# Optimization experiments

Hardware: AMD Instinct MI355X
Metric: run time of the kernel (lower is better)

## Reference

```python
import jax, jax.numpy as jnp
import numpy as np

N = 50000      # nodes
E = 800000     # edges
P = 200000     # link pairs
D_IN = 128     # input_dim
F_NUM = 128    # filter_num
OUT = 2        # out_dim
K = 10         # APPNP propagation steps
ALPHA = 0.1    # teleport prob


def setup_inputs() -> dict:
    key = jax.random.key(0)
    ks = jax.random.split(key, 9)
    x = jax.random.normal(ks[0], (N, D_IN), dtype=jnp.float32)
    edge_index = jax.random.randint(ks[1], (2, E), 0, N)
    index = jax.random.randint(ks[2], (P, 2), 0, N)
    s1 = 1.0 / np.sqrt(D_IN)
    s2 = 1.0 / np.sqrt(F_NUM)
    s3 = 1.0 / np.sqrt(2 * F_NUM)
    W1 = jax.random.uniform(ks[3], (F_NUM, D_IN), minval=-s1, maxval=s1)
    b1 = jax.random.uniform(ks[4], (F_NUM,), minval=-s1, maxval=s1)
    W2 = jax.random.uniform(ks[5], (F_NUM, F_NUM), minval=-s2, maxval=s2)
    b2 = jax.random.uniform(ks[6], (F_NUM,), minval=-s2, maxval=s2)
    W3 = jax.random.uniform(ks[7], (OUT, 2 * F_NUM), minval=-s3, maxval=s3)
    b3 = jax.random.uniform(ks[8], (OUT,), minval=-s3, maxval=s3)
    return {"x": x, "edge_index": edge_index, "index": index,
            "W1": W1, "b1": b1, "W2": W2, "b2": b2, "W3": W3, "b3": b3}


def _gcn_norm(edge_index, num_nodes):
    # PyG gcn_norm: add self-loops, sym norm D^{-1/2} (A+I) D^{-1/2}
    src, dst = edge_index[0], edge_index[1]
    loop = jnp.arange(num_nodes, dtype=src.dtype)
    src = jnp.concatenate([src, loop])
    dst = jnp.concatenate([dst, loop])
    deg = jax.ops.segment_sum(jnp.ones_like(src, dtype=jnp.float32), dst,
                              num_segments=num_nodes)
    dinv = jnp.where(deg > 0, jax.lax.rsqrt(deg), 0.0)
    norm = dinv[src] * dinv[dst]  # [E+N]
    return src, dst, norm


def _appnp(x, src, dst, norm, num_nodes):
    # h_{k+1} = (1-alpha) * A_hat h_k + alpha * x0
    def step(h, _):
        agg = jax.ops.segment_sum(norm[:, None] * h[src], dst,
                                  num_segments=num_nodes)
        return (1.0 - ALPHA) * agg + ALPHA * x, None
    h, _ = jax.lax.scan(step, x, None, length=K)
    return h


def reference(x, edge_index, index, W1, b1, W2, b2, W3, b3):
    num_nodes = x.shape[0]
    src, dst, norm = _gcn_norm(edge_index, num_nodes)
    h = x @ W1.T + b1                      # [N, F]
    h = jax.nn.relu(_appnp(h, src, dst, norm, num_nodes))
    h = h @ W2.T + b2                      # [N, F]
    h = jax.nn.relu(_appnp(h, src, dst, norm, num_nodes))
    feat = jnp.concatenate([h[index[:, 0]], h[index[:, 1]]], axis=-1)  # [P, 2F]
    out = feat @ W3.T + b3                 # [P, OUT]
    return jax.nn.log_softmax(out, axis=1)
```

## Files before the change

### kernel.cpp

```cpp
#include <hip/hip_runtime.h>
#include <math.h>

#define NN 50000
#define NE 800000
#define NP 200000
#define NF 128
#define NEDGE_TOT (NE + NN)
#define NBLK 196
#define NBK 64
#define DPB 782
#define BKCAP 16384
#define EPB 2048

typedef __attribute__((ext_vector_type(8))) short short8;
typedef __attribute__((ext_vector_type(4))) float float4v;
typedef __attribute__((ext_vector_type(2))) _Float16 h2;

__device__ __forceinline__ float bf_lo(unsigned u) { return __uint_as_float(u << 16); }
__device__ __forceinline__ float bf_hi(unsigned u) { return __uint_as_float(u & 0xffff0000u); }
__device__ __forceinline__ unsigned short f2bf(float f) {
    unsigned u = __float_as_uint(f);
    return (unsigned short)((u + 0x7fffu + ((u >> 16) & 1u)) >> 16);
}
__device__ __forceinline__ unsigned pack2bf(float a, float b) {
    return (unsigned)f2bf(a) | ((unsigned)f2bf(b) << 16);
}

__device__ __forceinline__ h2 u2h2(unsigned u) {
    union { unsigned u; h2 h; } c; c.u = u; return c.h;
}
__device__ __forceinline__ unsigned h22u(h2 h) {
    union { unsigned u; h2 h; } c; c.h = h; return c.u;
}
__device__ __forceinline__ float h_lo(unsigned u) { return (float)u2h2(u).x; }
__device__ __forceinline__ float h_hi(unsigned u) { return (float)u2h2(u).y; }
__device__ __forceinline__ unsigned pack2h(float a, float b) {
    h2 h; h.x = (_Float16)a; h.y = (_Float16)b; return h22u(h);
}

__global__ __launch_bounds__(256) void init_cnt_k(int* __restrict__ cnt) {
    int i = blockIdx.x * 256 + threadIdx.x;
    if (i < NN) cnt[i] = 1;
}

__global__ __launch_bounds__(256) void count_k(const int* __restrict__ ei,
                                               int* __restrict__ cnt) {
    int e = blockIdx.x * 256 + threadIdx.x;
    if (e < NE) atomicAdd(&cnt[ei[NE + e]], 1);
}

__global__ __launch_bounds__(256) void scan_reduce_k(const int* __restrict__ cnt,
                                                     int* __restrict__ bsum,
                                                     float* __restrict__ dinv) {
    __shared__ int s[256];
    int t = threadIdx.x;
    int idx = blockIdx.x * 256 + t;
    int v = (idx < NN) ? cnt[idx] : 0;
    if (idx < NN) dinv[idx] = rsqrtf((float)v);
    s[t] = v;
    __syncthreads();
    for (int off = 128; off > 0; off >>= 1) {
        if (t < off) s[t] += s[t + off];
        __syncthreads();
    }
    if (t == 0) bsum[blockIdx.x] = s[0];
}

__global__ __launch_bounds__(256) void scan_bsums_k(const int* __restrict__ bsum,
                                                    int* __restrict__ boff) {
    __shared__ int s[256];
    int t = threadIdx.x;
    int v = (t < NBLK) ? bsum[t] : 0;
    s[t] = v;
    __syncthreads();
    for (int off = 1; off < 256; off <<= 1) {
        int add = (t >= off) ? s[t - off] : 0;
        __syncthreads();
        s[t] += add;
        __syncthreads();
    }
    if (t < NBLK) boff[t] = s[t] - v;
}

__global__ __launch_bounds__(256) void scan_down_k(const int* __restrict__ cnt,
                                                   const int* __restrict__ boff,
                                                   int* __restrict__ row_ptr) {
    __shared__ int s[256];
    int t = threadIdx.x;
    int idx = blockIdx.x * 256 + t;
    int v = (idx < NN) ? cnt[idx] : 0;
    s[t] = v;
    __syncthreads();
    for (int off = 1; off < 256; off <<= 1) {
        int add = (t >= off) ? s[t - off] : 0;
        __syncthreads();
        s[t] += add;
        __syncthreads();
    }
    int excl = s[t] - v + boff[blockIdx.x];
    if (idx < NN) {
        row_ptr[idx] = excl;
        if (idx == NN - 1) row_ptr[NN] = excl + v;
    }
}

__global__ __launch_bounds__(256) void bin_k(const int* __restrict__ ei,
                                             int* __restrict__ gtail,
                                             int2* __restrict__ gbk) {
    __shared__ int cntA[NBK], baseA[NBK], gposA[NBK];
    __shared__ int2 stage[EPB];
    int tid = threadIdx.x;
    int ebase = blockIdx.x * EPB;
    int sv[8], dv[8], lp8[8], bk8[8];
    bool val[8];
    if (tid < NBK) cntA[tid] = 0;
    __syncthreads();
#pragma unroll
    for (int k = 0; k < 8; ++k) {
        int e = ebase + k * 256 + tid;
        val[k] = (e < NEDGE_TOT);
        if (val[k]) {
            int s, d;
            if (e < NE) { s = ei[e]; d = ei[NE + e]; }
            else        { s = d = e - NE; }
            sv[k] = s; dv[k] = d;
            bk8[k] = d / DPB;
            lp8[k] = atomicAdd(&cntA[bk8[k]], 1);
        }
    }
    __syncthreads();
    if (tid == 0) {
        int run = 0;
        for (int b = 0; b < NBK; ++b) { baseA[b] = run; run += cntA[b]; }
    }
    __syncthreads();
    if (tid < NBK && cntA[tid] > 0)
        gposA[tid] = atomicAdd(&gtail[tid], cntA[tid]);
    __syncthreads();
#pragma unroll
    for (int k = 0; k < 8; ++k)
        if (val[k]) {
            int2 r; r.x = sv[k]; r.y = dv[k];
            stage[baseA[bk8[k]] + lp8[k]] = r;
        }
    __syncthreads();
    int total = baseA[NBK - 1] + cntA[NBK - 1];
    for (int i = tid; i < total; i += 256) {
        int2 r = stage[i];
        int b = r.y / DPB;
        gbk[(size_t)b * BKCAP + gposA[b] + (i - baseA[b])] = r;
    }
}

__global__ __launch_bounds__(256) void build_k(const int* __restrict__ row_ptr,
                                               const int* __restrict__ gtail,
                                               const int2* __restrict__ gbk,
                                               int* __restrict__ cols) {
    __shared__ int wcur[DPB];
    int tid = threadIdx.x;
    int b = blockIdx.x;
    int d0 = b * DPB;
    for (int i = tid; i < DPB; i += 256) {
        int d = d0 + i;
        wcur[i] = (d < NN) ? row_ptr[d] : 0;
    }
    __syncthreads();
    int nb = gtail[b];
    const int2* src = gbk + (size_t)b * BKCAP;
    for (int t = tid; t < nb; t += 256) {
        int2 r = src[t];
        int pos = atomicAdd(&wcur[r.y - d0], 1);
        cols[pos] = r.x;
    }
}

__global__ __launch_bounds__(256) void zero_k(unsigned short* Ys1, unsigned short* Ys2,
                                              unsigned short* HA, unsigned short* HB,
                                              int* gtail) {
    int t = threadIdx.x;
    unsigned short* bufs[4] = {Ys1, Ys2, HA, HB};
    unsigned short* b = bufs[t >> 6];
    ((unsigned*)(b + (size_t)NN * NF))[t & 63] = 0u;
    if (t < NBK) gtail[t] = 0;
}

__global__ __launch_bounds__(256) void cast_w_k(const float* __restrict__ W,
                                                unsigned short* __restrict__ Wb) {
    int t = blockIdx.x * 256 + threadIdx.x;
    if (t >= 128 * 128 / 8) return;
    int i = t * 8;
    float4 f0 = *(const float4*)(W + i);
    float4 f1 = *(const float4*)(W + i + 4);
    uint4 q;
    q.x = pack2bf(f0.x, f0.y);
    q.y = pack2bf(f0.z, f0.w);
    q.z = pack2bf(f1.x, f1.y);
    q.w = pack2bf(f1.z, f1.w);
    *(uint4*)(Wb + i) = q;
}

#define GPAD 136
template <bool F32IN>
__global__ __launch_bounds__(256) void gemm_mfma_k(const void* __restrict__ Xv,
                                                   const unsigned short* __restrict__ Wb,
                                                   const float* __restrict__ bias,
                                                   const float* __restrict__ dinv,
                                                   unsigned short* __restrict__ Yu,
                                                   unsigned short* __restrict__ Ys,
                                                   int nrows) {
    __shared__ unsigned short sm[4 * 16 * GPAD];
    int wave = threadIdx.x >> 6, lane = threadIdx.x & 63;
    int rbase = blockIdx.x * 64 + wave * 16;
    if (rbase >= nrows) return;
    int quad = lane >> 4, mn = lane & 15;
    float4v acc[8];
#pragma unroll
    for (int ft = 0; ft < 8; ++ft) acc[ft] = (float4v){0.f, 0.f, 0.f, 0.f};
#pragma unroll
    for (int kb = 0; kb < 128; kb += 32) {
        short8 a;
        if (F32IN) {
            const float* X = (const float*)Xv;
            float4 f0 = *(const float4*)(X + (size_t)(rbase + mn) * NF + kb + quad * 8);
            float4 f1 = *(const float4*)(X + (size_t)(rbase + mn) * NF + kb + quad * 8 + 4);
            a[0] = (short)f2bf(f0.x); a[1] = (short)f2bf(f0.y);
            a[2] = (short)f2bf(f0.z); a[3] = (short)f2bf(f0.w);
            a[4] = (short)f2bf(f1.x); a[5] = (short)f2bf(f1.y);
            a[6] = (short)f2bf(f1.z); a[7] = (short)f2bf(f1.w);
        } else {
            const unsigned short* X = (const unsigned short*)Xv;
            a = *(const short8*)(X + (size_t)(rbase + mn) * NF + kb + quad * 8);
        }
#pragma unroll
        for (int ft = 0; ft < 8; ++ft) {
            short8 b = *(const short8*)(Wb + (size_t)(ft * 16 + mn) * NF + kb + quad * 8);
            acc[ft] = __builtin_amdgcn_mfma_f32_16x16x32_bf16(a, b, acc[ft], 0, 0, 0);
        }
    }
    unsigned short* smw = sm + wave * 16 * GPAD;
#pragma unroll
    for (int ft = 0; ft < 8; ++ft) {
        float bv = bias[ft * 16 + mn];
#pragma unroll
        for (int r = 0; r < 4; ++r) {
            union { _Float16 h; unsigned short s; } cv;
            cv.h = (_Float16)(acc[ft][r] + bv);
            smw[(quad * 4 + r) * GPAD + ft * 16 + mn] = cv.s;
        }
    }
    __syncthreads();
#pragma unroll
    for (int t = 0; t < 4; ++t) {
        int rl = t * 4 + quad;
        int row = rbase + rl;
        uint4 q = *(const uint4*)(smw + rl * GPAD + mn * 8);
        *(uint4*)(Yu + (size_t)row * NF + mn * 8) = q;
        float g = dinv[row];
        uint4 qs;
        qs.x = pack2h(g * h_lo(q.x), g * h_hi(q.x));
        qs.y = pack2h(g * h_lo(q.y), g * h_hi(q.y));
        qs.z = pack2h(g * h_lo(q.z), g * h_hi(q.z));
        qs.w = pack2h(g * h_lo(q.w), g * h_hi(q.w));
        *(uint4*)(Ys + (size_t)row * NF + mn * 8) = qs;
    }
}

__global__ __launch_bounds__(256) void appnp_h_k(const unsigned short* __restrict__ hs,
                                                 const unsigned short* __restrict__ x0,
                                                 const float* __restrict__ dinv,
                                                 unsigned short* __restrict__ out,
                                                 const int* __restrict__ row_ptr,
                                                 const int* __restrict__ cols,
                                                 int mode,
                                                 const float* __restrict__ W3,
                                                 float4* __restrict__ puv) {
    int wid = (blockIdx.x * 256 + threadIdx.x) >> 6;
    int lane = threadIdx.x & 63;
    if (wid >= NN) return;
    int half = lane >> 5, li = lane & 31;
    int beg = row_ptr[wid], end = row_ptr[wid + 1];
    h2 a01; a01.x = (_Float16)0.f; a01.y = (_Float16)0.f;
    h2 a23 = a01;
    for (int e = beg; e < end; e += 64) {
        int m = end - e;
        if (m > 64) m = 64;
        int c = (lane < m) ? cols[e + lane] : NN;
        for (int j = 0; j < m; j += 8) {
            int c0 = __shfl(c, j + half, 64);
            int c1 = __shfl(c, j + 2 + half, 64);
            int c2 = __shfl(c, j + 4 + half, 64);
            int c3 = __shfl(c, j + 6 + half, 64);
            uint2 q0 = *((const uint2*)(hs + (size_t)c0 * NF) + li);
            uint2 q1 = *((const uint2*)(hs + (size_t)c1 * NF) + li);
            uint2 q2 = *((const uint2*)(hs + (size_t)c2 * NF) + li);
            uint2 q3 = *((const uint2*)(hs + (size_t)c3 * NF) + li);
            a01 += (u2h2(q0.x) + u2h2(q1.x)) + (u2h2(q2.x) + u2h2(q3.x));
            a23 += (u2h2(q0.y) + u2h2(q1.y)) + (u2h2(q2.y) + u2h2(q3.y));
        }
    }
    a01 += u2h2((unsigned)__shfl_xor((int)h22u(a01), 32, 64));
    a23 += u2h2((unsigned)__shfl_xor((int)h22u(a23), 32, 64));
    if (half != 0) return;
    float g = dinv[wid];
    float s9 = 0.9f * g;
    uint2 xq = *((const uint2*)(x0 + (size_t)wid * NF) + li);
    float h0 = s9 * (float)a01.x + 0.1f * h_lo(xq.x);
    float h1 = s9 * (float)a01.y + 0.1f * h_hi(xq.x);
    float h2v = s9 * (float)a23.x + 0.1f * h_lo(xq.y);
    float h3 = s9 * (float)a23.y + 0.1f * h_hi(xq.y);
    if (mode == 0) {
        uint2 oq;
        oq.x = pack2h(g * h0, g * h1);
        oq.y = pack2h(g * h2v, g * h3);
        *((uint2*)(out + (size_t)wid * NF) + li) = oq;
    } else {
        h0 = fmaxf(h0, 0.f); h1 = fmaxf(h1, 0.f);
        h2v = fmaxf(h2v, 0.f); h3 = fmaxf(h3, 0.f);
        if (mode == 1) {
            uint2 oq;
            oq.x = pack2bf(h0, h1);
            oq.y = pack2bf(h2v, h3);
            *((uint2*)(out + (size_t)wid * NF) + li) = oq;
        } else {
            int fb = li * 4;
            float4 wu0 = *(const float4*)(W3 + fb);
            float4 wv0 = *(const float4*)(W3 + 128 + fb);
            float4 wu1 = *(const float4*)(W3 + 256 + fb);
            float4 wv1 = *(const float4*)(W3 + 384 + fb);
            float du0 = h0 * wu0.x + h1 * wu0.y + h2v * wu0.z + h3 * wu0.w;
            float du1 = h0 * wu1.x + h1 * wu1.y + h2v * wu1.z + h3 * wu1.w;
            float dv0 = h0 * wv0.x + h1 * wv0.y + h2v * wv0.z + h3 * wv0.w;
            float dv1 = h0 * wv1.x + h1 * wv1.y + h2v * wv1.z + h3 * wv1.w;
#pragma unroll
            for (int off = 1; off < 32; off <<= 1) {
                du0 += __shfl_xor(du0, off, 64);
                du1 += __shfl_xor(du1, off, 64);
                dv0 += __shfl_xor(dv0, off, 64);
                dv1 += __shfl_xor(dv1, off, 64);
            }
            if (li == 0) puv[wid] = make_float4(du0, du1, dv0, dv1);
        }
    }
}

__global__ __launch_bounds__(256) void pair2_k(const float4* __restrict__ puv,
                                               const int2* __restrict__ index,
                                               const float* __restrict__ b3,
                                               float* __restrict__ outp) {
    int p = blockIdx.x * 256 + threadIdx.x;
    if (p >= NP) return;
    int2 uv = index[p];
    float4 a = puv[uv.x];
    float4 b = puv[uv.y];
    float s0 = a.x + b.z + b3[0];
    float s1 = a.y + b.w + b3[1];
    float m = fmaxf(s0, s1);
    float lse = m + logf(expf(s0 - m) + expf(s1 - m));
    *(float2*)(outp + (size_t)p * 2) = make_float2(s0 - lse, s1 - lse);
}

extern "C" void kernel_launch(void* const* d_in, const int* in_sizes, int n_in,
                              void* d_out, int out_size, void* d_ws, size_t ws_size,
                              hipStream_t stream) {
    const float* x  = (const float*)d_in[0];
    const int* ei   = (const int*)d_in[1];
    const int* idx  = (const int*)d_in[2];
    const float* W1 = (const float*)d_in[3];
    const float* b1 = (const float*)d_in[4];
    const float* W2 = (const float*)d_in[5];
    const float* b2 = (const float*)d_in[6];
    const float* W3 = (const float*)d_in[7];
    const float* b3 = (const float*)d_in[8];
    float* out = (float*)d_out;

    char* ws = (char*)d_ws;
    size_t off = 0;
    auto alloc = [&](size_t bytes) -> void* {
        void* p = ws + off;
        off = (off + bytes + 255) & ~(size_t)255;
        return p;
    };
    const size_t HROWS = (size_t)(NN + 1) * NF;
    int*   cnt     = (int*)  alloc(NN * sizeof(int));
    float* dinv    = (float*)alloc(NN * sizeof(float));
    int*   row_ptr = (int*)  alloc((NN + 1) * sizeof(int));
    int*   bsum    = (int*)  alloc(NBLK * sizeof(int));
    int*   boff    = (int*)  alloc(NBLK * sizeof(int));
    int*   gtail   = (int*)  alloc(NBK * sizeof(int));
    int2*  gbk     = (int2*) alloc((size_t)NBK * BKCAP * sizeof(int2));
    int*   cols    = (int*)  alloc((size_t)NEDGE_TOT * sizeof(int));
    float4* puv    = (float4*)alloc((size_t)NN * sizeof(float4));
    unsigned short* Wb1 = (unsigned short*)alloc(128 * 128 * 2);
    unsigned short* Wb2 = (unsigned short*)alloc(128 * 128 * 2);
    unsigned short* Yu1 = (unsigned short*)alloc(HROWS * 2);
    unsigned short* Ys1 = (unsigned short*)alloc(HROWS * 2);
    unsigned short* Yu2 = (unsigned short*)alloc(HROWS * 2);
    unsigned short* Ys2 = (unsigned short*)alloc(HROWS * 2);
    unsigned short* HA  = (unsigned short*)alloc(HROWS * 2);
    unsigned short* HB  = (unsigned short*)alloc(HROWS * 2);
    unsigned short* Hrelu = (unsigned short*)alloc((size_t)NN * NF * 2);

    const int gN    = (NN + 255) / 256;
    const int gE    = (NE + 255) / 256;
    const int gBin  = (NEDGE_TOT + EPB - 1) / EPB;
    const int gGemm = (NN + 63) / 64;
    const int gStep = (NN * 64 + 255) / 256;
    const int gPair = (NP + 255) / 256;

    cast_w_k<<<8, 256, 0, stream>>>(W1, Wb1);
    cast_w_k<<<8, 256, 0, stream>>>(W2, Wb2);
    zero_k<<<1, 256, 0, stream>>>(Ys1, Ys2, HA, HB, gtail);
    init_cnt_k<<<gN, 256, 0, stream>>>(cnt);
    count_k<<<gE, 256, 0, stream>>>(ei, cnt);
    scan_reduce_k<<<NBLK, 256, 0, stream>>>(cnt, bsum, dinv);
    scan_bsums_k<<<1, 256, 0, stream>>>(bsum, boff);
    scan_down_k<<<NBLK, 256, 0, stream>>>(cnt, boff, row_ptr);
    bin_k<<<gBin, 256, 0, stream>>>(ei, gtail, gbk);
    build_k<<<NBK, 256, 0, stream>>>(row_ptr, gtail, gbk, cols);

    gemm_mfma_k<true><<<gGemm, 256, 0, stream>>>(x, Wb1, b1, dinv, Yu1, Ys1, NN);
    {
        const unsigned short* cur = Ys1;
        for (int k = 0; k < 10; ++k) {
            unsigned short* dst = (k == 9) ? Hrelu : ((k & 1) ? HB : HA);
            appnp_h_k<<<gStep, 256, 0, stream>>>(cur, Yu1, dinv, dst, row_ptr,
                                                 cols, (k == 9) ? 1 : 0, W3, puv);
            cur = dst;
        }
    }
    gemm_mfma_k<false><<<gGemm, 256, 0, stream>>>(Hrelu, Wb2, b2, dinv, Yu2, Ys2, NN);
    {
        const unsigned short* cur = Ys2;
        for (int k = 0; k < 10; ++k) {
            unsigned short* dst = (k & 1) ? HB : HA;
            appnp_h_k<<<gStep, 256, 0, stream>>>(cur, Yu2, dinv, dst, row_ptr,
                                                 cols, (k == 9) ? 2 : 0, W3, puv);
            cur = dst;
        }
    }
    pair2_k<<<gPair, 256, 0, stream>>>(puv, (const int2*)idx, b3, out);
}
```

Baseline: 825.9 us.

## Split feature matrices into 16-wide column slices for cache-local APPNP gathers

Result: slower. 2.284 ms (+176.5%).

```diff
diff --git a/kernel.cpp b/kernel.cpp
--- a/kernel.cpp
+++ b/kernel.cpp
@@ -5,12 +5,15 @@
 #define NE 800000
 #define NP 200000
 #define NF 128
+#define NNP (NN + 1)
 #define NEDGE_TOT (NE + NN)
 #define NBLK 196
 #define NBK 64
 #define DPB 782
 #define BKCAP 16384
 #define EPB 2048
+#define NSL 8
+#define SF 16
 
 typedef __attribute__((ext_vector_type(8))) short short8;
 typedef __attribute__((ext_vector_type(4))) float float4v;
@@ -38,9 +41,13 @@
     h2 h; h.x = (_Float16)a; h.y = (_Float16)b; return h22u(h);
 }
 
-__global__ __launch_bounds__(256) void init_cnt_k(int* __restrict__ cnt) {
+__global__ __launch_bounds__(256) void init_cnt_k(int* __restrict__ cnt,
+                                                  float4* __restrict__ puv) {
     int i = blockIdx.x * 256 + threadIdx.x;
-    if (i < NN) cnt[i] = 1;
+    if (i < NN) {
+        cnt[i] = 1;
+        puv[i] = make_float4(0.f, 0.f, 0.f, 0.f);
+    }
 }
 
 __global__ __launch_bounds__(256) void count_k(const int* __restrict__ ei,
@@ -155,7 +162,7 @@
 __global__ __launch_bounds__(256) void build_k(const int* __restrict__ row_ptr,
                                                const int* __restrict__ gtail,
                                                const int2* __restrict__ gbk,
-                                               int* __restrict__ cols) {
+                                               unsigned short* __restrict__ cols) {
     __shared__ int wcur[DPB];
     int tid = threadIdx.x;
     int b = blockIdx.x;
@@ -170,7 +177,7 @@
     for (int t = tid; t < nb; t += 256) {
         int2 r = src[t];
         int pos = atomicAdd(&wcur[r.y - d0], 1);
-        cols[pos] = r.x;
+        cols[pos] = (unsigned short)r.x;
     }
 }
 
@@ -179,8 +186,9 @@
                                               int* gtail) {
     int t = threadIdx.x;
     unsigned short* bufs[4] = {Ys1, Ys2, HA, HB};
-    unsigned short* b = bufs[t >> 6];
-    ((unsigned*)(b + (size_t)NN * NF))[t & 63] = 0u;
+    unsigned short* bp = bufs[t >> 6];
+    int s = (t >> 3) & 7, u = t & 7;
+    ((unsigned*)(bp + (size_t)(s * NNP + NN) * SF))[u] = 0u;
     if (t < NBK) gtail[t] = 0;
 }
 
@@ -254,56 +262,61 @@
         int rl = t * 4 + quad;
         int row = rbase + rl;
         uint4 q = *(const uint4*)(smw + rl * GPAD + mn * 8);
-        *(uint4*)(Yu + (size_t)row * NF + mn * 8) = q;
+        size_t sb = ((size_t)(mn >> 1) * NNP + row) * SF + (mn & 1) * 8;
+        *(uint4*)(Yu + sb) = q;
         float g = dinv[row];
         uint4 qs;
         qs.x = pack2h(g * h_lo(q.x), g * h_hi(q.x));
         qs.y = pack2h(g * h_lo(q.y), g * h_hi(q.y));
         qs.z = pack2h(g * h_lo(q.z), g * h_hi(q.z));
         qs.w = pack2h(g * h_lo(q.w), g * h_hi(q.w));
-        *(uint4*)(Ys + (size_t)row * NF + mn * 8) = qs;
-    }
-}
-
-__global__ __launch_bounds__(256) void appnp_h_k(const unsigned short* __restrict__ hs,
-                                                 const unsigned short* __restrict__ x0,
-                                                 const float* __restrict__ dinv,
-                                                 unsigned short* __restrict__ out,
-                                                 const int* __restrict__ row_ptr,
-                                                 const int* __restrict__ cols,
-                                                 int mode,
-                                                 const float* __restrict__ W3,
-                                                 float4* __restrict__ puv) {
-    int wid = (blockIdx.x * 256 + threadIdx.x) >> 6;
-    int lane = threadIdx.x & 63;
+        *(uint4*)(Ys + sb) = qs;
+    }
+}
+
+__global__ __launch_bounds__(1024) void appnp_slice_k(
+    const unsigned short* __restrict__ hs,
+    const unsigned short* __restrict__ x0,
+    const float* __restrict__ dinv,
+    unsigned short* __restrict__ out,
+    const int* __restrict__ row_ptr,
+    const unsigned short* __restrict__ cols,
+    int mode,
+    const float* __restrict__ W3,
+    float* __restrict__ puv) {
+    int b = blockIdx.x;
+    int s = b & 7;
+    int wave = threadIdx.x >> 6, lane = threadIdx.x & 63;
+    int wid = (b >> 3) * 16 + wave;
     if (wid >= NN) return;
-    int half = lane >> 5, li = lane & 31;
+    int rg = lane >> 2, fo = lane & 3;
+    const unsigned short* hsS = hs + (size_t)s * NNP * SF;
     int beg = row_ptr[wid], end = row_ptr[wid + 1];
     h2 a01; a01.x = (_Float16)0.f; a01.y = (_Float16)0.f;
     h2 a23 = a01;
     for (int e = beg; e < end; e += 64) {
         int m = end - e;
         if (m > 64) m = 64;
-        int c = (lane < m) ? cols[e + lane] : NN;
-        for (int j = 0; j < m; j += 8) {
-            int c0 = __shfl(c, j + half, 64);
-            int c1 = __shfl(c, j + 2 + half, 64);
-            int c2 = __shfl(c, j + 4 + half, 64);
-            int c3 = __shfl(c, j + 6 + half, 64);
-            uint2 q0 = *((const uint2*)(hs + (size_t)c0 * NF) + li);
-            uint2 q1 = *((const uint2*)(hs + (size_t)c1 * NF) + li);
-            uint2 q2 = *((const uint2*)(hs + (size_t)c2 * NF) + li);
-            uint2 q3 = *((const uint2*)(hs + (size_t)c3 * NF) + li);
-            a01 += (u2h2(q0.x) + u2h2(q1.x)) + (u2h2(q2.x) + u2h2(q3.x));
-            a23 += (u2h2(q0.y) + u2h2(q1.y)) + (u2h2(q2.y) + u2h2(q3.y));
-        }
-    }
+        int c = (lane < m) ? (int)cols[e + lane] : NN;
+        for (int j = 0; j < m; j += 16) {
+            int cr = __shfl(c, j + rg, 64);
+            uint2 q = *(const uint2*)(hsS + (size_t)cr * SF + fo * 4);
+            a01 += u2h2(q.x);
+            a23 += u2h2(q.y);
+        }
+    }
+    a01 += u2h2((unsigned)__shfl_xor((int)h22u(a01), 4, 64));
+    a23 += u2h2((unsigned)__shfl_xor((int)h22u(a23), 4, 64));
+    a01 += u2h2((unsigned)__shfl_xor((int)h22u(a01), 8, 64));
+    a23 += u2h2((unsigned)__shfl_xor((int)h22u(a23), 8, 64));
+    a01 += u2h2((unsigned)__shfl_xor((int)h22u(a01), 16, 64));
+    a23 += u2h2((unsigned)__shfl_xor((int)h22u(a23), 16, 64));
     a01 += u2h2((unsigned)__shfl_xor((int)h22u(a01), 32, 64));
     a23 += u2h2((unsigned)__shfl_xor((int)h22u(a23), 32, 64));
-    if (half != 0) return;
+    if (lane >= 4) return;
     float g = dinv[wid];
     float s9 = 0.9f * g;
-    uint2 xq = *((const uint2*)(x0 + (size_t)wid * NF) + li);
+    uint2 xq = *(const uint2*)(x0 + ((size_t)s * NNP + wid) * SF + fo * 4);
     float h0 = s9 * (float)a01.x + 0.1f * h_lo(xq.x);
     float h1 = s9 * (float)a01.y + 0.1f * h_hi(xq.x);
     float h2v = s9 * (float)a23.x + 0.1f * h_lo(xq.y);
@@ -312,7 +325,7 @@
         uint2 oq;
         oq.x = pack2h(g * h0, g * h1);
         oq.y = pack2h(g * h2v, g * h3);
-        *((uint2*)(out + (size_t)wid * NF) + li) = oq;
+        *(uint2*)(out + ((size_t)s * NNP + wid) * SF + fo * 4) = oq;
     } else {
         h0 = fmaxf(h0, 0.f); h1 = fmaxf(h1, 0.f);
         h2v = fmaxf(h2v, 0.f); h3 = fmaxf(h3, 0.f);
@@ -320,9 +333,9 @@
             uint2 oq;
             oq.x = pack2bf(h0, h1);
             oq.y = pack2bf(h2v, h3);
-            *((uint2*)(out + (size_t)wid * NF) + li) = oq;
+            *(uint2*)(out + (size_t)wid * NF + s * SF + fo * 4) = oq;
         } else {
-            int fb = li * 4;
+            int fb = s * SF + fo * 4;
             float4 wu0 = *(const float4*)(W3 + fb);
             float4 wv0 = *(const float4*)(W3 + 128 + fb);
             float4 wu1 = *(const float4*)(W3 + 256 + fb);
@@ -331,14 +344,12 @@
             float du1 = h0 * wu1.x + h1 * wu1.y + h2v * wu1.z + h3 * wu1.w;
             float dv0 = h0 * wv0.x + h1 * wv0.y + h2v * wv0.z + h3 * wv0.w;
             float dv1 = h0 * wv1.x + h1 * wv1.y + h2v * wv1.z + h3 * wv1.w;
-#pragma unroll
-            for (int off = 1; off < 32; off <<= 1) {
-                du0 += __shfl_xor(du0, off, 64);
-                du1 += __shfl_xor(du1, off, 64);
-                dv0 += __shfl_xor(dv0, off, 64);
-                dv1 += __shfl_xor(dv1, off, 64);
-            }
-            if (li == 0) puv[wid] = make_float4(du0, du1, dv0, dv1);
+            du0 += __shfl_xor(du0, 1, 64); du0 += __shfl_xor(du0, 2, 64);
+            du1 += __shfl_xor(du1, 1, 64); du1 += __shfl_xor(du1, 2, 64);
+            dv0 += __shfl_xor(dv0, 1, 64); dv0 += __shfl_xor(dv0, 2, 64);
+            dv1 += __shfl_xor(dv1, 1, 64); dv1 += __shfl_xor(dv1, 2, 64);
+            float v = (fo == 0) ? du0 : (fo == 1) ? du1 : (fo == 2) ? dv0 : dv1;
+            atomicAdd(&puv[(size_t)wid * 4 + fo], v);
         }
     }
 }
@@ -380,7 +391,7 @@
         off = (off + bytes + 255) & ~(size_t)255;
         return p;
     };
-    const size_t HROWS = (size_t)(NN + 1) * NF;
+    const size_t HROWS = (size_t)NSL * NNP * SF;
     int*   cnt     = (int*)  alloc(NN * sizeof(int));
     float* dinv    = (float*)alloc(NN * sizeof(float));
     int*   row_ptr = (int*)  alloc((NN + 1) * sizeof(int));
@@ -388,7 +399,7 @@
     int*   boff    = (int*)  alloc(NBLK * sizeof(int));
     int*   gtail   = (int*)  alloc(NBK * sizeof(int));
     int2*  gbk     = (int2*) alloc((size_t)NBK * BKCAP * sizeof(int2));
-    int*   cols    = (int*)  alloc((size_t)NEDGE_TOT * sizeof(int));
+    unsigned short* cols = (unsigned short*)alloc((size_t)NEDGE_TOT * 2);
     float4* puv    = (float4*)alloc((size_t)NN * sizeof(float4));
     unsigned short* Wb1 = (unsigned short*)alloc(128 * 128 * 2);
     unsigned short* Wb2 = (unsigned short*)alloc(128 * 128 * 2);
@@ -404,13 +415,13 @@
     const int gE    = (NE + 255) / 256;
     const int gBin  = (NEDGE_TOT + EPB - 1) / EPB;
     const int gGemm = (NN + 63) / 64;
-    const int gStep = (NN * 64 + 255) / 256;
+    const int gSlice = (NN / 16) * NSL;
     const int gPair = (NP + 255) / 256;
 
     cast_w_k<<<8, 256, 0, stream>>>(W1, Wb1);
     cast_w_k<<<8, 256, 0, stream>>>(W2, Wb2);
     zero_k<<<1, 256, 0, stream>>>(Ys1, Ys2, HA, HB, gtail);
-    init_cnt_k<<<gN, 256, 0, stream>>>(cnt);
+    init_cnt_k<<<gN, 256, 0, stream>>>(cnt, puv);
     count_k<<<gE, 256, 0, stream>>>(ei, cnt);
     scan_reduce_k<<<NBLK, 256, 0, stream>>>(cnt, bsum, dinv);
     scan_bsums_k<<<1, 256, 0, stream>>>(bsum, boff);
@@ -418,13 +429,14 @@
     bin_k<<<gBin, 256, 0, stream>>>(ei, gtail, gbk);
     build_k<<<NBK, 256, 0, stream>>>(row_ptr, gtail, gbk, cols);
 
+    float* puvf = (float*)puv;
     gemm_mfma_k<true><<<gGemm, 256, 0, stream>>>(x, Wb1, b1, dinv, Yu1, Ys1, NN);
     {
         const unsigned short* cur = Ys1;
         for (int k = 0; k < 10; ++k) {
             unsigned short* dst = (k == 9) ? Hrelu : ((k & 1) ? HB : HA);
-            appnp_h_k<<<gStep, 256, 0, stream>>>(cur, Yu1, dinv, dst, row_ptr,
-                                                 cols, (k == 9) ? 1 : 0, W3, puv);
+            appnp_slice_k<<<gSlice, 1024, 0, stream>>>(cur, Yu1, dinv, dst, row_ptr,
+                                                       cols, (k == 9) ? 1 : 0, W3, puvf);
             cur = dst;
         }
     }
@@ -433,8 +445,8 @@
         const unsigned short* cur = Ys2;
         for (int k = 0; k < 10; ++k) {
             unsigned short* dst = (k & 1) ? HB : HA;
-            appnp_h_k<<<gStep, 256, 0, stream>>>(cur, Yu2, dinv, dst, row_ptr,
-                                                 cols, (k == 9) ? 2 : 0, W3, puv);
+            appnp_slice_k<<<gSlice, 1024, 0, stream>>>(cur, Yu2, dinv, dst, row_ptr,
+                                                       cols, (k == 9) ? 2 : 0, W3, puvf);
             cur = dst;
         }
     }
```
